# Kernel optimization log

Measured on AMD Instinct MI355X. Metric: run time of the kernel, lower is better.

Reference implementation:

```python
import jax, jax.numpy as jnp
import numpy as np
from jax import lax


def setup_inputs() -> dict:
    key = jax.random.key(0)
    k1, k2 = jax.random.split(key)
    B, T, D, O = 8, 8192, 512, 512
    x = jax.random.normal(k1, (B, T, D), dtype=jnp.float32)
    # Dense kernel over concat([h_t, state]) -> width 2*D
    W = jax.random.normal(k2, (2 * D, O), dtype=jnp.float32) * (1.0 / np.sqrt(2 * D))
    b = jnp.zeros((O,), dtype=jnp.float32)
    decay = jnp.float32(0.95)
    return {"x": x, "W": W, "b": b, "decay": decay}


def reference(x, W, b, decay):
    # x: [B, T, D]; W: [2D, O]; b: [O]; decay: scalar lambda
    B, T, D = x.shape
    lam = jnp.clip(decay, 0.5, 0.999)  # keras constraint on the decay weight
    h_avg = jnp.mean(x, axis=0)  # [T, D] batch-mean per timestep

    # EMA recurrence: s_t = lam * s_{t-1} + (1 - lam) * h_avg_t, s_{-1} = 0
    def step(s, a):
        s = lam * s + (1.0 - lam) * a
        return s, s

    _, states = lax.scan(step, jnp.zeros((D,), x.dtype), h_avg)  # [T, D]

    # proj(concat([h_t, s_t])) = h_t @ W_h + s_t @ W_s + b (fused, no concat materialized)
    W_h, W_s = W[:D], W[D:]
    out = jnp.einsum('btd,do->bto', x, W_h) + jnp.einsum('td,do->to', states, W_s)[None] + b
    return out  # [B, T, O]
```

## Files before the change

kernel.cpp:

```cpp
#include <hip/hip_runtime.h>
#include <hip/hip_bf16.h>
#include <stdint.h>

#define T_DIM 8192
#define B_DIM 8
#define D_DIM 512
#define O_DIM 512

typedef __attribute__((ext_vector_type(4))) float f32x4;
typedef __attribute__((ext_vector_type(8))) short short8;
typedef __attribute__((ext_vector_type(4))) unsigned short us4;

__device__ __forceinline__ unsigned short f2bf(float f) {
  union { float f; uint32_t u; } v; v.f = f;
  uint32_t u = v.u + 0x7FFFu + ((v.u >> 16) & 1u);
  return (unsigned short)(u >> 16);
}

__device__ __forceinline__ void gload_lds16(const void* g, void* l) {
  __builtin_amdgcn_global_load_lds(
      (const __attribute__((address_space(1))) void*)g,
      (__attribute__((address_space(3))) void*)l, 16, 0, 0);
}

__device__ __forceinline__ float clip_lam(const float* decay) {
  return fminf(fmaxf(decay[0], 0.5f), 0.999f);
}

__global__ void mean_cvt_kernel(const float* __restrict__ x, float* __restrict__ havg,
                                unsigned short* __restrict__ xbf) {
  int idx = blockIdx.x * 256 + threadIdx.x;
  const f32x4* x4 = (const f32x4*)x;
  us4* xb4 = (us4*)xbf;
  const size_t stride = (size_t)T_DIM * D_DIM / 4;
  f32x4 v[8];
#pragma unroll
  for (int b = 0; b < B_DIM; ++b) v[b] = x4[(size_t)b * stride + idx];
  us4 o[8];
#pragma unroll
  for (int b = 0; b < B_DIM; ++b)
#pragma unroll
    for (int j = 0; j < 4; ++j) o[b][j] = f2bf(v[b][j]);
#pragma unroll
  for (int b = 0; b < B_DIM; ++b) xb4[(size_t)b * stride + idx] = o[b];
  f32x4 s = ((v[0] + v[1]) + (v[2] + v[3])) + ((v[4] + v[5]) + (v[6] + v[7]));
  s *= 0.125f;
  ((f32x4*)havg)[idx] = s;
}

__global__ void wconv_kernel(const float* __restrict__ W, unsigned short* __restrict__ Wt) {
  __shared__ float tile[64][65];
  int bk = blockIdx.x >> 3;
  int bn = blockIdx.x & 7;
  int tr = threadIdx.x >> 4;
  int tc = threadIdx.x & 15;
#pragma unroll
  for (int i = 0; i < 4; ++i) {
    int row = i * 16 + tr;
    f32x4 v = *(const f32x4*)&W[(size_t)(bk * 64 + row) * O_DIM + bn * 64 + tc * 4];
#pragma unroll
    for (int j = 0; j < 4; ++j) tile[row][tc * 4 + j] = v[j];
  }
  __syncthreads();
#pragma unroll
  for (int i = 0; i < 4; ++i) {
    int nl = i * 16 + tr;
    us4 o;
#pragma unroll
    for (int j = 0; j < 4; ++j) o[j] = f2bf(tile[tc * 4 + j][nl]);
    int kg = bk * 64 + tc * 4;
    int h = kg >> 9;
    int k = kg & 511;
    *(us4*)&Wt[(size_t)h * (512 * 512) + (size_t)(bn * 64 + nl) * 512 + k] = o;
  }
}

#define CHUNK 128
#define NCHUNK (T_DIM / CHUNK)

__global__ void scanA_kernel(float* __restrict__ havg, const float* __restrict__ decay) {
  int chunk = blockIdx.x >> 1;
  int d = ((blockIdx.x & 1) << 8) + threadIdx.x;
  float lam = clip_lam(decay);
  float om = 1.0f - lam;
  size_t base = (size_t)chunk * CHUNK * D_DIM + d;
  float cur[16], nxt[16];
#pragma unroll
  for (int i = 0; i < 16; ++i) cur[i] = havg[base + (size_t)i * D_DIM];
  float s = 0.f;
  for (int blk = 0; blk < 8; ++blk) {
    if (blk < 7) {
#pragma unroll
      for (int i = 0; i < 16; ++i)
        nxt[i] = havg[base + (size_t)((blk + 1) * 16 + i) * D_DIM];
    }
#pragma unroll
    for (int i = 0; i < 16; ++i) {
      s = lam * s + om * cur[i];
      havg[base + (size_t)(blk * 16 + i) * D_DIM] = s;
    }
#pragma unroll
    for (int i = 0; i < 16; ++i) cur[i] = nxt[i];
  }
}

__global__ void scanB_kernel(const float* __restrict__ havg, const float* __restrict__ decay,
                             float* __restrict__ carry) {
  int d = blockIdx.x * 256 + threadIdx.x;
  float lam = clip_lam(decay);
  float l2 = lam * lam;
  float l4 = l2 * l2;
  float l8 = l4 * l4;
  float l16 = l8 * l8;
  float l32 = l16 * l16;
  float l64 = l32 * l32;
  float l128 = l64 * l64;
  float e[NCHUNK];
#pragma unroll
  for (int c = 0; c < NCHUNK; ++c)
    e[c] = havg[((size_t)c * CHUNK + CHUNK - 1) * D_DIM + d];
  float s = 0.f;
#pragma unroll
  for (int c = 0; c < NCHUNK; ++c) {
    s = l128 * s + e[c];
    carry[c * D_DIM + d] = s;
  }
}

__global__ void scanC_kernel(const float* __restrict__ havg, const float* __restrict__ carry,
                             const float* __restrict__ decay, unsigned short* __restrict__ st) {
  int idx = blockIdx.x * 256 + threadIdx.x;
  int t = idx >> 7;
  int d4 = idx & 127;
  int c = t >> 7;
  int k = t & 127;
  float lam = clip_lam(decay);
  float w = exp2f((float)(k + 1) * __log2f(lam));
  f32x4 p = ((const f32x4*)havg)[idx];
  f32x4 cin = {0.f, 0.f, 0.f, 0.f};
  if (c > 0) cin = ((const f32x4*)carry)[(size_t)(c - 1) * 128 + d4];
  us4 o;
#pragma unroll
  for (int j = 0; j < 4; ++j) o[j] = f2bf(p[j] + w * cin[j]);
  ((us4*)st)[idx] = o;
}

template <bool ADD_SBAR>
__global__ __launch_bounds__(256, 4)
void gemm128bf(const unsigned short* __restrict__ A, const unsigned short* __restrict__ Bt,
               const float* __restrict__ extra, float* __restrict__ C) {
  __shared__ __align__(16) char smem[2][16384];

  int nwg = gridDim.x;
  int bid = blockIdx.x;
  int swz = (bid & 7) * (nwg >> 3) + (bid >> 3);
  int tm = swz >> 2, tn = swz & 3;
  int brow = tm << 7, bcol = tn << 7;

  int tid = threadIdx.x;
  int wave = tid >> 6, lane = tid & 63;
  int wr = (wave >> 1) << 6, wc = (wave & 1) << 6;
  const int lr = lane & 15, lkb = lane >> 4;

  const int soct = ((lane & 3) ^ ((lane >> 3) & 3)) << 3;
  const int pm = (lr >> 1) & 3;

  const size_t a_base = (size_t)(brow + (wave << 4) + (lane >> 2)) * 512 + soct;
  const size_t b_base = (size_t)(bcol + (wave << 4) + (lane >> 2)) * 512 + soct;

  f32x4 acc[4][4];
#pragma unroll
  for (int m = 0; m < 4; ++m)
#pragma unroll
    for (int n = 0; n < 4; ++n) acc[m][n] = (f32x4){0.f, 0.f, 0.f, 0.f};

#define STAGE(buf, kt_)                                                        \
  {                                                                            \
    int k0_ = (kt_) << 5;                                                      \
    _Pragma("unroll")                                                          \
    for (int it = 0; it < 2; ++it)                                             \
      gload_lds16(A + a_base + (size_t)(it << 15) + k0_,                       \
                  &smem[buf][(((it << 2) + wave) << 10)]);                     \
    _Pragma("unroll")                                                          \
    for (int it = 0; it < 2; ++it)                                             \
      gload_lds16(Bt + b_base + (size_t)(it << 15) + k0_,                      \
                  &smem[buf][8192 + (((it << 2) + wave) << 10)]);              \
  }

  STAGE(0, 0);

#pragma unroll 2
  for (int kt = 0; kt < 16; ++kt) {
    const int cur = kt & 1;
    if (kt < 15) {
      STAGE(cur ^ 1, kt + 1);
      asm volatile("s_waitcnt vmcnt(4)" ::: "memory");
    } else {
      asm volatile("s_waitcnt vmcnt(0)" ::: "memory");
    }
    __builtin_amdgcn_s_barrier();
    __builtin_amdgcn_sched_barrier(0);

    const unsigned short* As = (const unsigned short*)&smem[cur][0];
    const unsigned short* Bs = (const unsigned short*)&smem[cur][8192];
    short8 af[4], bfr[4];
#pragma unroll
    for (int m = 0; m < 4; ++m)
      af[m] = *(const short8*)(As + (size_t)(wr + (m << 4) + lr) * 32 + ((lkb ^ pm) << 3));
#pragma unroll
    for (int n = 0; n < 4; ++n)
      bfr[n] = *(const short8*)(Bs + (size_t)(wc + (n << 4) + lr) * 32 + ((lkb ^ pm) << 3));

#pragma unroll
    for (int m = 0; m < 4; ++m)
#pragma unroll
      for (int n = 0; n < 4; ++n)
        acc[m][n] = __builtin_amdgcn_mfma_f32_16x16x32_bf16(af[m], bfr[n], acc[m][n], 0, 0, 0);

    __builtin_amdgcn_sched_barrier(0);
    __builtin_amdgcn_s_barrier();
  }
#undef STAGE

  float* tp = (float*)&smem[0][0] + (size_t)wave * 2048;
#pragma unroll
  for (int m = 0; m < 4; ++m) {
#pragma unroll
    for (int n = 0; n < 4; ++n)
#pragma unroll
      for (int j = 0; j < 4; ++j)
        tp[((lkb << 2) + j) * 68 + (n << 4) + lr] = acc[m][n][j];
    __syncthreads();
#pragma unroll
    for (int p = 0; p < 4; ++p) {
      int rl = (p << 2) + (lane >> 4);
      int c0 = (lane & 15) << 2;
      f32x4 v = *(const f32x4*)(tp + rl * 68 + c0);
      int row = brow + wr + (m << 4) + rl;
      int col = bcol + wc + c0;
      f32x4 e;
      if constexpr (ADD_SBAR)
        e = *(const f32x4*)&extra[(size_t)(row & (T_DIM - 1)) * O_DIM + col];
      else
        e = *(const f32x4*)&extra[col];
      v += e;
      *(f32x4*)&C[(size_t)row * O_DIM + col] = v;
    }
    __syncthreads();
  }
}

extern "C" void kernel_launch(void* const* d_in, const int* in_sizes, int n_in,
                              void* d_out, int out_size, void* d_ws, size_t ws_size,
                              hipStream_t stream) {
  (void)in_sizes; (void)n_in; (void)out_size; (void)ws_size;
  const float* x     = (const float*)d_in[0];
  const float* W     = (const float*)d_in[1];
  const float* bias  = (const float*)d_in[2];
  const float* decay = (const float*)d_in[3];
  float* out = (float*)d_out;

  char* ws = (char*)d_ws;
  size_t off = 0;
  float*          havg  = (float*)(ws + off);          off += 16777216;
  unsigned short* st    = (unsigned short*)(ws + off); off += 8388608;
  unsigned short* Wt    = (unsigned short*)(ws + off); off += 1048576;
  float*          sbar  = (float*)(ws + off);          off += 16777216;
  float*          carry = (float*)(ws + off);          off += 131072;
  unsigned short* xbf   = (unsigned short*)(ws + off); off += (size_t)B_DIM * T_DIM * D_DIM * 2;

  mean_cvt_kernel<<<T_DIM * D_DIM / 4 / 256, 256, 0, stream>>>(x, havg, xbf);
  wconv_kernel<<<128, 256, 0, stream>>>(W, Wt);
  scanA_kernel<<<NCHUNK * 2, 256, 0, stream>>>(havg, decay);
  scanB_kernel<<<2, 256, 0, stream>>>(havg, decay, carry);
  scanC_kernel<<<T_DIM * D_DIM / 4 / 256, 256, 0, stream>>>(havg, carry, decay, st);
  gemm128bf<false><<<(T_DIM / 128) * 4, 256, 0, stream>>>(st, Wt + 512 * 512, bias, sbar);
  gemm128bf<true><<<(B_DIM * T_DIM / 128) * 4, 256, 0, stream>>>(xbf, Wt, sbar, out);
}
```

Measured before the change: 136.2 us.

## Fuse fp32-to-bf16 conversion of x into the main GEMM A-tile load

The mean kernel no longer writes a bf16 copy of x. A new GEMM variant reads fp32 x directly into registers, converts it with packed bf16 conversion instructions, and stores it into swizzled LDS, while B still streams via global_load_lds. This removes a 64MB bf16 write and its 64MB re-read. In exchange the GEMM reads twice the A bytes (fp32), and the A-tile staging now goes through registers, which raises register pressure and may stall the pipeline. x is read once by the mean kernel and again by the GEMM.

```diff
diff --git a/kernel.cpp b/kernel.cpp
--- a/kernel.cpp
+++ b/kernel.cpp
@@ -10,6 +10,7 @@
 typedef __attribute__((ext_vector_type(4))) float f32x4;
 typedef __attribute__((ext_vector_type(8))) short short8;
 typedef __attribute__((ext_vector_type(4))) unsigned short us4;
+typedef __attribute__((ext_vector_type(4))) uint32_t u32x4;
 
 __device__ __forceinline__ unsigned short f2bf(float f) {
   union { float f; uint32_t u; } v; v.f = f;
@@ -17,6 +18,12 @@
   return (unsigned short)(u >> 16);
 }
 
+__device__ __forceinline__ uint32_t cvtpk(float a, float b) {
+  uint32_t r;
+  asm("v_cvt_pk_bf16_f32 %0, %1, %2" : "=v"(r) : "v"(a), "v"(b));
+  return r;
+}
+
 __device__ __forceinline__ void gload_lds16(const void* g, void* l) {
   __builtin_amdgcn_global_load_lds(
       (const __attribute__((address_space(1))) void*)g,
@@ -27,22 +34,13 @@
   return fminf(fmaxf(decay[0], 0.5f), 0.999f);
 }
 
-__global__ void mean_cvt_kernel(const float* __restrict__ x, float* __restrict__ havg,
-                                unsigned short* __restrict__ xbf) {
+__global__ void mean_kernel(const float* __restrict__ x, float* __restrict__ havg) {
   int idx = blockIdx.x * 256 + threadIdx.x;
   const f32x4* x4 = (const f32x4*)x;
-  us4* xb4 = (us4*)xbf;
   const size_t stride = (size_t)T_DIM * D_DIM / 4;
   f32x4 v[8];
 #pragma unroll
   for (int b = 0; b < B_DIM; ++b) v[b] = x4[(size_t)b * stride + idx];
-  us4 o[8];
-#pragma unroll
-  for (int b = 0; b < B_DIM; ++b)
-#pragma unroll
-    for (int j = 0; j < 4; ++j) o[b][j] = f2bf(v[b][j]);
-#pragma unroll
-  for (int b = 0; b < B_DIM; ++b) xb4[(size_t)b * stride + idx] = o[b];
   f32x4 s = ((v[0] + v[1]) + (v[2] + v[3])) + ((v[4] + v[5]) + (v[6] + v[7]));
   s *= 0.125f;
   ((f32x4*)havg)[idx] = s;
@@ -145,7 +143,6 @@
   ((us4*)st)[idx] = o;
 }
 
-template <bool ADD_SBAR>
 __global__ __launch_bounds__(256, 4)
 void gemm128bf(const unsigned short* __restrict__ A, const unsigned short* __restrict__ Bt,
                const float* __restrict__ extra, float* __restrict__ C) {
@@ -238,11 +235,121 @@
       f32x4 v = *(const f32x4*)(tp + rl * 68 + c0);
       int row = brow + wr + (m << 4) + rl;
       int col = bcol + wc + c0;
-      f32x4 e;
-      if constexpr (ADD_SBAR)
-        e = *(const f32x4*)&extra[(size_t)(row & (T_DIM - 1)) * O_DIM + col];
-      else
-        e = *(const f32x4*)&extra[col];
+      f32x4 e = *(const f32x4*)&extra[col];
+      v += e;
+      *(f32x4*)&C[(size_t)row * O_DIM + col] = v;
+    }
+    __syncthreads();
+  }
+}
+
+__global__ __launch_bounds__(256, 4)
+void gemm128xf(const float* __restrict__ X, const unsigned short* __restrict__ Bt,
+               const float* __restrict__ extra, float* __restrict__ C) {
+  __shared__ __align__(16) char smem[2][16384];
+
+  int nwg = gridDim.x;
+  int bid = blockIdx.x;
+  int swz = (bid & 7) * (nwg >> 3) + (bid >> 3);
+  int tm = swz >> 2, tn = swz & 3;
+  int brow = tm << 7, bcol = tn << 7;
+
+  int tid = threadIdx.x;
+  int wave = tid >> 6, lane = tid & 63;
+  int wr = (wave >> 1) << 6, wc = (wave & 1) << 6;
+  const int lr = lane & 15, lkb = lane >> 4;
+  const int pm = (lr >> 1) & 3;
+
+  const int arow = tid >> 1, ahalf = tid & 1;
+  const float* agp = X + (size_t)(brow + arow) * 512 + (ahalf << 4);
+  const int aperm = (arow >> 1) & 3;
+  const int aw0 = arow * 64 + (((ahalf << 1) ^ aperm) << 4);
+  const int aw1 = aw0 ^ 16;
+
+  const int soct = ((lane & 3) ^ ((lane >> 3) & 3)) << 3;
+  const size_t b_base = (size_t)(bcol + (wave << 4) + (lane >> 2)) * 512 + soct;
+
+  f32x4 acc[4][4];
+#pragma unroll
+  for (int m = 0; m < 4; ++m)
+#pragma unroll
+    for (int n = 0; n < 4; ++n) acc[m][n] = (f32x4){0.f, 0.f, 0.f, 0.f};
+
+  f32x4 a0, a1, a2, a3;
+#define ALOAD(kt_)                                                             \
+  {                                                                            \
+    const float* p_ = agp + ((kt_) << 5);                                      \
+    a0 = *(const f32x4*)p_;       a1 = *(const f32x4*)(p_ + 4);                \
+    a2 = *(const f32x4*)(p_ + 8); a3 = *(const f32x4*)(p_ + 12);               \
+  }
+#define BSTAGE(buf, kt_)                                                       \
+  {                                                                            \
+    int k0_ = (kt_) << 5;                                                      \
+    _Pragma("unroll")                                                          \
+    for (int it = 0; it < 2; ++it)                                             \
+      gload_lds16(Bt + b_base + (size_t)(it << 15) + k0_,                      \
+                  &smem[buf][8192 + (((it << 2) + wave) << 10)]);              \
+  }
+#define AWRITE(buf)                                                            \
+  {                                                                            \
+    u32x4 w0_ = {cvtpk(a0[0], a0[1]), cvtpk(a0[2], a0[3]),                     \
+                 cvtpk(a1[0], a1[1]), cvtpk(a1[2], a1[3])};                    \
+    u32x4 w1_ = {cvtpk(a2[0], a2[1]), cvtpk(a2[2], a2[3]),                     \
+                 cvtpk(a3[0], a3[1]), cvtpk(a3[2], a3[3])};                    \
+    *(u32x4*)&smem[buf][aw0] = w0_;                                            \
+    *(u32x4*)&smem[buf][aw1] = w1_;                                            \
+  }
+
+  ALOAD(0); BSTAGE(0, 0);
+  AWRITE(0);
+  __syncthreads();
+
+#pragma unroll 2
+  for (int kt = 0; kt < 16; ++kt) {
+    const int cur = kt & 1;
+    if (kt < 15) { ALOAD(kt + 1); BSTAGE(cur ^ 1, kt + 1); }
+    __builtin_amdgcn_sched_barrier(0);
+
+    const unsigned short* As = (const unsigned short*)&smem[cur][0];
+    const unsigned short* Bs = (const unsigned short*)&smem[cur][8192];
+    short8 af[4], bfr[4];
+#pragma unroll
+    for (int m = 0; m < 4; ++m)
+      af[m] = *(const short8*)(As + (size_t)(wr + (m << 4) + lr) * 32 + ((lkb ^ pm) << 3));
+#pragma unroll
+    for (int n = 0; n < 4; ++n)
+      bfr[n] = *(const short8*)(Bs + (size_t)(wc + (n << 4) + lr) * 32 + ((lkb ^ pm) << 3));
+
+#pragma unroll
+    for (int m = 0; m < 4; ++m)
+#pragma unroll
+      for (int n = 0; n < 4; ++n)
+        acc[m][n] = __builtin_amdgcn_mfma_f32_16x16x32_bf16(af[m], bfr[n], acc[m][n], 0, 0, 0);
+
+    if (kt < 15) AWRITE(cur ^ 1);
+    __syncthreads();
+  }
+#undef ALOAD
+#undef BSTAGE
+#undef AWRITE
+
+  float* tp = (float*)&smem[0][0] + (size_t)wave * 2048;
+#pragma unroll
+  for (int m = 0; m < 4; ++m) {
+#pragma unroll
+    for (int n = 0; n < 4; ++n)
+#pragma unroll
+      for (int j = 0; j < 4; ++j)
+        tp[((lkb << 2) + j) * 68 + (n << 4) + lr] = acc[m][n][j];
+    __syncthreads();
+#pragma unroll
+    for (int p = 0; p < 4; ++p) {
+      int rl = (p << 2) + (lane >> 4);
+      int c0 = (lane & 15) << 2;
+      f32x4 v = *(const f32x4*)(tp + rl * 68 + c0);
+      int row = brow + wr + (m << 4) + rl;
+      int col = bcol + wc + c0;
+      f32x4 e = *(const f32x4*)&extra[(size_t)(row & (T_DIM - 1)) * O_DIM + col];
       v += e;
       *(f32x4*)&C[(size_t)row * O_DIM + col] = v;
     }
@@ -267,13 +374,12 @@
   unsigned short* Wt    = (unsigned short*)(ws + off); off += 1048576;
   float*          sbar  = (float*)(ws + off);          off += 16777216;
   float*          carry = (float*)(ws + off);          off += 131072;
-  unsigned short* xbf   = (unsigned short*)(ws + off); off += (size_t)B_DIM * T_DIM * D_DIM * 2;
-
-  mean_cvt_kernel<<<T_DIM * D_DIM / 4 / 256, 256, 0, stream>>>(x, havg, xbf);
+
+  mean_kernel<<<T_DIM * D_DIM / 4 / 256, 256, 0, stream>>>(x, havg);
   wconv_kernel<<<128, 256, 0, stream>>>(W, Wt);
   scanA_kernel<<<NCHUNK * 2, 256, 0, stream>>>(havg, decay);
   scanB_kernel<<<2, 256, 0, stream>>>(havg, decay, carry);
   scanC_kernel<<<T_DIM * D_DIM / 4 / 256, 256, 0, stream>>>(havg, carry, decay, st);
-  gemm128bf<false><<<(T_DIM / 128) * 4, 256, 0, stream>>>(st, Wt + 512 * 512, bias, sbar);
-  gemm128bf<true><<<(B_DIM * T_DIM / 128) * 4, 256, 0, stream>>>(xbf, Wt, sbar, out);
-}
+  gemm128bf<<<(T_DIM / 128) * 4, 256, 0, stream>>>(st, Wt + 512 * 512, bias, sbar);
+  gemm128xf<<<(B_DIM * T_DIM / 128) * 4, 256, 0, stream>>>(x, Wt, sbar, out);
+}
```

Measured after the change: 129.8 us. 4.7% less time.
